# Optimization experiments

Hardware: AMD Instinct MI355X
Metric: run time of the kernel (lower is better)

## Reference

```python
import jax, jax.numpy as jnp
import numpy as np


def setup_inputs() -> dict:
    key = jax.random.key(0)
    ks = jax.random.split(key, 8)
    N, DIN, DOUT = 8192, 1024, 1024
    s = 1.0 / np.sqrt(DIN)
    return {
        "gAB": jax.random.normal(ks[0], (N, DIN), dtype=jnp.float32),
        "gAG": jax.random.normal(ks[1], (N, DIN), dtype=jnp.float32),
        "Wab": jax.random.normal(ks[2], (DIN, DOUT), dtype=jnp.float32) * s,
        "Wag": jax.random.normal(ks[3], (DIN, DOUT), dtype=jnp.float32) * s,
        "bab": jax.random.normal(ks[4], (DOUT,), dtype=jnp.float32) * 0.01,
        "bag": jax.random.normal(ks[5], (DOUT,), dtype=jnp.float32) * 0.01,
        "sAB": jax.random.normal(ks[6], (N, DOUT), dtype=jnp.float32),
        "sAG": jax.random.normal(ks[7], (N, DOUT), dtype=jnp.float32),
    }


def reference(gAB, gAG, Wab, Wag, bab, bag, sAB, sAG) -> jnp.ndarray:
    # project() per encoder (Linear): [N, DIN] @ [DIN, DOUT] + b
    pAB = gAB @ Wab + bab  # [N, DOUT]
    pAG = gAG @ Wag + bag  # [N, DOUT]
    # torch.diag(pAB @ pAG.T) == row-wise dot product (avoids O(N^2 d) waste)
    h1 = jnp.sum(pAB * pAG, axis=1, keepdims=True)  # [N, 1]
    h2 = jnp.sum(sAB * sAG, axis=1, keepdims=True)  # [N, 1]
    # mean over concatenated (h1, h2) columns, keepdim=True
    h = jnp.mean(jnp.concatenate([h1, h2], axis=1), axis=1, keepdims=True)  # [N, 1]
    return h
```

## Files before the change

kernel.cpp:

```cpp
#include <hip/hip_runtime.h>
#include <hip/hip_bf16.h>
#include <stdint.h>

typedef __attribute__((ext_vector_type(8))) short bf16x8;
typedef __attribute__((ext_vector_type(4))) float f32x4;

#define DIN 1024
#define NROWS 8192

__device__ __forceinline__ unsigned short f2bf(float f) {
    union { float f; unsigned u; } v; v.f = f;
    unsigned r = v.u + 0x7FFFu + ((v.u >> 16) & 1u);
    return (unsigned short)(r >> 16);
}

__device__ __forceinline__ int fswz(int r) { return (r ^ (r >> 2)) & 3; }

__device__ __forceinline__ size_t swz_byte(int R, int c) {
    return ((size_t)R * DIN + (size_t)(c & ~31)) * 2
         + (size_t)((((c >> 3) & 3) ^ fswz(R)) << 4)
         + (size_t)((c & 7) * 2);
}

__device__ __forceinline__ void gload_lds16(const void* g, void* l) {
    __builtin_amdgcn_global_load_lds(
        (const __attribute__((address_space(1))) unsigned*)g,
        (__attribute__((address_space(3))) unsigned*)l, 16, 0, 0);
}

__global__ __launch_bounds__(256) void prep_kernel(const float* __restrict__ Wab,
                                                   const float* __restrict__ Wag,
                                                   const float* __restrict__ bab,
                                                   const float* __restrict__ bag,
                                                   float* __restrict__ ws_f,
                                                   unsigned short* __restrict__ Whab,
                                                   unsigned short* __restrict__ Whag) {
    int b = blockIdx.x;
    int wave = threadIdx.x >> 6, lane = threadIdx.x & 63;
    if (b == 256) {
        if (wave == 0) {
            float acc = 0.f;
            for (int j = lane; j < DIN; j += 64) acc += bab[j] * bag[j];
            for (int off = 32; off; off >>= 1) acc += __shfl_xor(acc, off);
            if (lane == 0) ws_f[2048] = acc;
        }
        return;
    }
    int r = b * 4 + wave;
    int fr = fswz(r);
    {
        const float* wrow = Wab + (size_t)r * DIN;
        char* hrow = (char*)Whab + (size_t)r * DIN * 2;
        float acc = 0.f;
#pragma unroll
        for (int it = 0; it < 4; ++it) {
            int col = it * 256 + lane * 4;
            float4 w = *reinterpret_cast<const float4*>(wrow + col);
            float4 bv = *reinterpret_cast<const float4*>(bag + col);
            acc += w.x * bv.x + w.y * bv.y + w.z * bv.z + w.w * bv.w;
            ushort4 h; h.x = f2bf(w.x); h.y = f2bf(w.y); h.z = f2bf(w.z); h.w = f2bf(w.w);
            *reinterpret_cast<ushort4*>(hrow + (col & ~31) * 2 + ((((col >> 3) & 3) ^ fr) << 4) + (col & 7) * 2) = h;
        }
        for (int off = 32; off; off >>= 1) acc += __shfl_xor(acc, off);
        if (lane == 0) ws_f[r] = acc;
    }
    {
        const float* wrow = Wag + (size_t)r * DIN;
        char* hrow = (char*)Whag + (size_t)r * DIN * 2;
        float acc = 0.f;
#pragma unroll
        for (int it = 0; it < 4; ++it) {
            int col = it * 256 + lane * 4;
            float4 w = *reinterpret_cast<const float4*>(wrow + col);
            float4 bv = *reinterpret_cast<const float4*>(bab + col);
            acc += w.x * bv.x + w.y * bv.y + w.z * bv.z + w.w * bv.w;
            ushort4 h; h.x = f2bf(w.x); h.y = f2bf(w.y); h.z = f2bf(w.z); h.w = f2bf(w.w);
            *reinterpret_cast<ushort4*>(hrow + (col & ~31) * 2 + ((((col >> 3) & 3) ^ fr) << 4) + (col & 7) * 2) = h;
        }
        for (int off = 32; off; off >>= 1) acc += __shfl_xor(acc, off);
        if (lane == 0) ws_f[1024 + r] = acc;
    }
}

__global__ __launch_bounds__(256) void combo_kernel(const unsigned short* __restrict__ Whag,
                                                    const unsigned short* __restrict__ Whab,
                                                    unsigned short* __restrict__ Mt,
                                                    const float* __restrict__ gAB,
                                                    const float* __restrict__ sAB,
                                                    const float* __restrict__ sAG,
                                                    const float* __restrict__ ws_f,
                                                    unsigned short* __restrict__ gABh,
                                                    float* __restrict__ out,
                                                    int writecast) {
    __shared__ unsigned short sm[2][2][2][2048];
    int b = blockIdx.x;
    int tid = threadIdx.x, wave = tid >> 6, lane = tid & 63;

    if (b < 256) {
        int grp = wave >> 1, w2 = wave & 1;
        int kg = lane >> 4, cl = lane & 15;
        int br = b >> 4, bc = b & 15;
        int u = tid & 127;

        const char* Abase = (const char*)Whag + ((size_t)(br * 64) * DIN + grp * 512) * 2;
        const char* Bbase = (const char*)Whab + ((size_t)(bc * 64) * DIN + grp * 512) * 2;

        int offA[2], offB[4];
#pragma unroll
        for (int m = 0; m < 2; ++m) { int row = w2 * 32 + m * 16 + cl; offA[m] = row * 32 + ((kg ^ fswz(row)) << 3); }
#pragma unroll
        for (int n = 0; n < 4; ++n) { int row = n * 16 + cl; offB[n] = row * 32 + ((kg ^ fswz(row)) << 3); }

        f32x4 acc[2][4] = {};
#define STAGE_MT(buf, t)                                                            \
        _Pragma("unroll")                                                           \
        for (int it = 0; it < 2; ++it) {                                            \
            int un = u + it * 128, urow = un >> 2, uc = un & 3;                     \
            gload_lds16(Abase + (size_t)urow * 2048 + (t) * 64 + uc * 16,           \
                        &sm[grp][buf][0][un * 8]);                                  \
            gload_lds16(Bbase + (size_t)urow * 2048 + (t) * 64 + uc * 16,           \
                        &sm[grp][buf][1][un * 8]);                                  \
        }
        STAGE_MT(0, 0);
        for (int t = 0; t < 16; ++t) {
            int p = t & 1;
            __syncthreads();
            if (t < 15) { STAGE_MT(p ^ 1, t + 1); }
            bf16x8 af[2], bfr[4];
#pragma unroll
            for (int m = 0; m < 2; ++m) af[m] = *reinterpret_cast<const bf16x8*>(&sm[grp][p][0][offA[m]]);
#pragma unroll
            for (int n = 0; n < 4; ++n) bfr[n] = *reinterpret_cast<const bf16x8*>(&sm[grp][p][1][offB[n]]);
            __builtin_amdgcn_s_setprio(1);
#pragma unroll
            for (int m = 0; m < 2; ++m)
#pragma unroll
                for (int n = 0; n < 4; ++n)
                    acc[m][n] = __builtin_amdgcn_mfma_f32_16x16x32_bf16(af[m], bfr[n], acc[m][n], 0, 0, 0);
            __builtin_amdgcn_s_setprio(0);
        }
#undef STAGE_MT
        __syncthreads();
        float* red = (float*)sm;
        if (grp == 1) {
#pragma unroll
            for (int m = 0; m < 2; ++m)
#pragma unroll
                for (int n = 0; n < 4; ++n)
#pragma unroll
                    for (int j = 0; j < 4; ++j)
                        red[(w2 * 32 + m * 16 + kg * 4 + j) * 68 + n * 16 + cl] = acc[m][n][j];
        }
        __syncthreads();
        if (grp == 0) {
#pragma unroll
            for (int m = 0; m < 2; ++m)
#pragma unroll
                for (int n = 0; n < 4; ++n)
#pragma unroll
                    for (int j = 0; j < 4; ++j) {
                        int rl = w2 * 32 + m * 16 + kg * 4 + j, cll = n * 16 + cl;
                        float v = acc[m][n][j] + red[rl * 68 + cll];
                        int R = br * 64 + rl, C = bc * 64 + cll;
                        *(unsigned short*)((char*)Mt + swz_byte(R, C)) = f2bf(v);
                    }
        }
        return;
    }

    int row = (b - 256) * 4 + wave;
    const float* ga = gAB + (size_t)row * DIN;
    const float* sa = sAB + (size_t)row * DIN;
    const float* sg = sAG + (size_t)row * DIN;
    char* gh = (char*)gABh + (size_t)row * DIN * 2;
    int fr = fswz(row);
    float acc = 0.f;
#pragma unroll
    for (int cc = 0; cc < 4; ++cc) {
        int col = cc * 256 + lane * 4;
        float4 a = *reinterpret_cast<const float4*>(ga + col);
        float4 x = *reinterpret_cast<const float4*>(sa + col);
        float4 y = *reinterpret_cast<const float4*>(sg + col);
        float4 v = *reinterpret_cast<const float4*>(ws_f + col);
        acc += x.x * y.x + x.y * y.y + x.z * y.z + x.w * y.w;
        acc += a.x * v.x + a.y * v.y + a.z * v.z + a.w * v.w;
        if (writecast) {
            ushort4 h; h.x = f2bf(a.x); h.y = f2bf(a.y); h.z = f2bf(a.z); h.w = f2bf(a.w);
            *reinterpret_cast<ushort4*>(gh + (col & ~31) * 2 + ((((col >> 3) & 3) ^ fr) << 4) + (col & 7) * 2) = h;
        }
    }
#pragma unroll
    for (int off = 32; off; off >>= 1) acc += __shfl_xor(acc, off);
    if (lane == 0) out[row] = 0.5f * (acc + ws_f[2048]);
}

template <int PRECAST, int KSPLIT>
__global__ __launch_bounds__(256, 4) void gemm_kernel(const float* __restrict__ gAB,
                                                      const unsigned short* __restrict__ gABh,
                                                      const float* __restrict__ gAG,
                                                      const unsigned short* __restrict__ Mt,
                                                      const float* __restrict__ ws_f,
                                                      float* __restrict__ out) {
    __shared__ unsigned short lds_a[2][128 * 32];
    __shared__ unsigned short lds_b[2][128 * 32];
    constexpr int KLEN = DIN / KSPLIT;
    constexpr int NSTEP = KLEN / 32;
    int b = blockIdx.x;
    int x = b & 7, s = b >> 3;
    int rblk = x + 8 * (s & 7);
    int u2 = s >> 3;
    int ks = u2 & (KSPLIT - 1);
    int cblk = u2 / KSPLIT;
    int tid = threadIdx.x, wave = tid >> 6, lane = tid & 63;
    int wr = wave >> 1, wc = wave & 1;
    int kg = lane >> 4, cl = lane & 15;
    int row0 = rblk * 128, col0 = cblk * 128;

    int offA[4], offB[4];
#pragma unroll
    for (int m = 0; m < 4; ++m) { int row = wr * 64 + m * 16 + cl; offA[m] = row * 32 + ((kg ^ fswz(row)) << 3); }
#pragma unroll
    for (int n = 0; n < 4; ++n) { int row = wc * 64 + n * 16 + cl; offB[n] = row * 32 + ((kg ^ fswz(row)) << 3); }

    size_t kofs = (size_t)(ks * KLEN) * 2;
    const char* Ab = (const char*)gABh + (size_t)row0 * DIN * 2 + kofs;
    const char* Bb = (const char*)Mt + (size_t)col0 * DIN * 2 + kofs;
    int u0 = tid, u1 = tid + 256;
    size_t a0 = (size_t)(u0 >> 2) * (DIN * 2) + (u0 & 3) * 16;
    size_t a1 = (size_t)(u1 >> 2) * (DIN * 2) + (u1 & 3) * 16;

    f32x4 acc[4][4] = {};
    float4 ra[4];
    if (PRECAST) {
        gload_lds16(Ab + a0, (char*)&lds_a[0][0] + u0 * 16);
        gload_lds16(Ab + a1, (char*)&lds_a[0][0] + u1 * 16);
        gload_lds16(Bb + a0, (char*)&lds_b[0][0] + u0 * 16);
        gload_lds16(Bb + a1, (char*)&lds_b[0][0] + u1 * 16);

        for (int t = 0; t < NSTEP; ++t) {
            int p = t & 1;
            __syncthreads();
            if (t < NSTEP - 1) {
                gload_lds16(Ab + a0 + (t + 1) * 64, (char*)&lds_a[p ^ 1][0] + u0 * 16);
                gload_lds16(Ab + a1 + (t + 1) * 64, (char*)&lds_a[p ^ 1][0] + u1 * 16);
                gload_lds16(Bb + a0 + (t + 1) * 64, (char*)&lds_b[p ^ 1][0] + u0 * 16);
                gload_lds16(Bb + a1 + (t + 1) * 64, (char*)&lds_b[p ^ 1][0] + u1 * 16);
            }
            bf16x8 af[4], bfr[4];
#pragma unroll
            for (int m = 0; m < 4; ++m) af[m] = *reinterpret_cast<const bf16x8*>(&lds_a[p][offA[m]]);
#pragma unroll
            for (int n = 0; n < 4; ++n) bfr[n] = *reinterpret_cast<const bf16x8*>(&lds_b[p][offB[n]]);
            __builtin_amdgcn_s_setprio(1);
#pragma unroll
            for (int m = 0; m < 4; ++m)
#pragma unroll
                for (int n = 0; n < 4; ++n)
                    acc[m][n] = __builtin_amdgcn_mfma_f32_16x16x32_bf16(af[m], bfr[n], acc[m][n], 0, 0, 0);
            __builtin_amdgcn_s_setprio(0);
        }
    } else {
#pragma unroll
        for (int it = 0; it < 4; ++it) {
            int u = tid + it * 256;
            ra[it] = *reinterpret_cast<const float4*>(gAB + (size_t)(row0 + (u >> 3)) * DIN + ks * KLEN + (u & 7) * 4);
        }
#pragma unroll
        for (int it = 0; it < 4; ++it) {
            int u = tid + it * 256, row = u >> 3, c4 = u & 7;
            ushort4 h; h.x = f2bf(ra[it].x); h.y = f2bf(ra[it].y); h.z = f2bf(ra[it].z); h.w = f2bf(ra[it].w);
            *reinterpret_cast<ushort4*>((char*)&lds_a[0][0] + row * 64 + ((((c4 >> 1) ^ fswz(row))) << 4) + (c4 & 1) * 8) = h;
        }
        gload_lds16(Bb + a0, (char*)&lds_b[0][0] + u0 * 16);
        gload_lds16(Bb + a1, (char*)&lds_b[0][0] + u1 * 16);
        for (int t = 0; t < NSTEP; ++t) {
            int p = t & 1;
            __syncthreads();
            if (t < NSTEP - 1) {
#pragma unroll
                for (int it = 0; it < 4; ++it) {
                    int u = tid + it * 256;
                    ra[it] = *reinterpret_cast<const float4*>(gAB + (size_t)(row0 + (u >> 3)) * DIN + ks * KLEN + (t + 1) * 32 + (u & 7) * 4);
                }
                gload_lds16(Bb + a0 + (t + 1) * 64, (char*)&lds_b[p ^ 1][0] + u0 * 16);
                gload_lds16(Bb + a1 + (t + 1) * 64, (char*)&lds_b[p ^ 1][0] + u1 * 16);
            }
            bf16x8 af[4], bfr[4];
#pragma unroll
            for (int m = 0; m < 4; ++m) af[m] = *reinterpret_cast<const bf16x8*>(&lds_a[p][offA[m]]);
#pragma unroll
            for (int n = 0; n < 4; ++n) bfr[n] = *reinterpret_cast<const bf16x8*>(&lds_b[p][offB[n]]);
#pragma unroll
            for (int m = 0; m < 4; ++m)
#pragma unroll
                for (int n = 0; n < 4; ++n)
                    acc[m][n] = __builtin_amdgcn_mfma_f32_16x16x32_bf16(af[m], bfr[n], acc[m][n], 0, 0, 0);
            if (t < NSTEP - 1) {
#pragma unroll
                for (int it = 0; it < 4; ++it) {
                    int u = tid + it * 256, row = u >> 3, c4 = u & 7;
                    ushort4 h; h.x = f2bf(ra[it].x); h.y = f2bf(ra[it].y); h.z = f2bf(ra[it].z); h.w = f2bf(ra[it].w);
                    *reinterpret_cast<ushort4*>((char*)&lds_a[p ^ 1][0] + row * 64 + ((((c4 >> 1) ^ fswz(row))) << 4) + (c4 & 1) * 8) = h;
                }
            }
        }
    }

    const float* vag = ws_f + 1024;
#pragma unroll
    for (int m = 0; m < 4; ++m)
#pragma unroll
        for (int j = 0; j < 4; ++j) {
            int row = row0 + wr * 64 + m * 16 + kg * 4 + j;
            const float* gr = gAG + (size_t)row * DIN;
            float t = 0.f;
#pragma unroll
            for (int n = 0; n < 4; ++n) {
                int col = col0 + wc * 64 + n * 16 + cl;
                float addv = (ks == 0) ? vag[col] : 0.f;
                t += gr[col] * (acc[m][n][j] + addv);
            }
            t += __shfl_xor(t, 1);
            t += __shfl_xor(t, 2);
            t += __shfl_xor(t, 4);
            t += __shfl_xor(t, 8);
            if (cl == 0) atomicAdd(out + row, 0.5f * t);
        }
}

extern "C" void kernel_launch(void* const* d_in, const int* in_sizes, int n_in,
                              void* d_out, int out_size, void* d_ws, size_t ws_size,
                              hipStream_t stream) {
    const float* gAB = (const float*)d_in[0];
    const float* gAG = (const float*)d_in[1];
    const float* Wab = (const float*)d_in[2];
    const float* Wag = (const float*)d_in[3];
    const float* bab = (const float*)d_in[4];
    const float* bag = (const float*)d_in[5];
    const float* sAB = (const float*)d_in[6];
    const float* sAG = (const float*)d_in[7];
    float* out = (float*)d_out;

    float* ws_f = (float*)d_ws;
    char* base = (char*)d_ws + 16384;
    unsigned short* Mt = (unsigned short*)base;
    unsigned short* Whag = (unsigned short*)(base + (size_t)2 * 1024 * 1024);
    unsigned short* Whab = (unsigned short*)(base + (size_t)4 * 1024 * 1024);
    unsigned short* gABh = (unsigned short*)(base + (size_t)6 * 1024 * 1024);
    size_t need_full = 16384 + (size_t)22 * 1024 * 1024;
    int precast = (ws_size >= need_full) ? 1 : 0;

    prep_kernel<<<257, 256, 0, stream>>>(Wab, Wag, bab, bag, ws_f, Whab, Whag);
    combo_kernel<<<2304, 256, 0, stream>>>(Whag, Whab, Mt, gAB, sAB, sAG, ws_f, gABh, out, precast);
    if (precast)
        gemm_kernel<1, 2><<<1024, 256, 0, stream>>>(gAB, gABh, gAG, Mt, ws_f, out);
    else
        gemm_kernel<0, 2><<<1024, 256, 0, stream>>>(gAB, gABh, gAG, Mt, ws_f, out);
}
```

Measured before the change: 61.46 us.

## Use 256x256 GEMM tiles with 512 threads and 4-way K split

Replaces the 128x128, 256-thread, 2-way K-split GEMM on the precast path with a 256x256 tile kernel that uses 8 waves and splits K four ways, with 512 blocks. Each wave computes a 128x64 sub-tile, loading A fragments per m-row so they are reused across four B fragments. The goal is higher operand reuse per LDS and global byte and less redundant global traffic. In exchange, LDS per block doubles (64KB), accumulator register pressure rises, and the larger K split doubles the atomic adds into the output. The fallback path is refactored into a separate kernel with macros.

```diff
diff --git a/kernel.cpp b/kernel.cpp
--- a/kernel.cpp
+++ b/kernel.cpp
@@ -194,17 +194,103 @@
     if (lane == 0) out[row] = 0.5f * (acc + ws_f[2048]);
 }
 
-template <int PRECAST, int KSPLIT>
-__global__ __launch_bounds__(256, 4) void gemm_kernel(const float* __restrict__ gAB,
-                                                      const unsigned short* __restrict__ gABh,
-                                                      const float* __restrict__ gAG,
-                                                      const unsigned short* __restrict__ Mt,
-                                                      const float* __restrict__ ws_f,
-                                                      float* __restrict__ out) {
+__global__ __launch_bounds__(512, 4) void gemm256k4(const unsigned short* __restrict__ gABh,
+                                                    const float* __restrict__ gAG,
+                                                    const unsigned short* __restrict__ Mt,
+                                                    const float* __restrict__ ws_f,
+                                                    float* __restrict__ out) {
+    __shared__ unsigned short lds_a[2][256 * 32];
+    __shared__ unsigned short lds_b[2][256 * 32];
+    constexpr int NSTEP = 8;
+    int b = blockIdx.x;
+    int x = b & 7, s = b >> 3;
+    int rblk = x + 8 * (s & 3);
+    int rem = s >> 2;
+    int ks = rem & 3;
+    int cblk = rem >> 2;
+    int tid = threadIdx.x, wave = tid >> 6, lane = tid & 63;
+    int wr = wave >> 2, wc = wave & 3;
+    int kg = lane >> 4, cl = lane & 15;
+    int row0 = rblk * 256, col0 = cblk * 256;
+
+    const char* Ab = (const char*)gABh + (size_t)row0 * 2048 + ks * 512;
+    const char* Bb = (const char*)Mt + (size_t)col0 * 2048 + ks * 512;
+
+    int offA[8], offB[4];
+#pragma unroll
+    for (int m = 0; m < 8; ++m) { int row = wr * 128 + m * 16 + cl; offA[m] = row * 64 + ((kg ^ fswz(row)) << 4); }
+#pragma unroll
+    for (int n = 0; n < 4; ++n) { int row = wc * 64 + n * 16 + cl; offB[n] = row * 64 + ((kg ^ fswz(row)) << 4); }
+
+#define STAGE(buf, t) do {                                                          \
+    _Pragma("unroll")                                                               \
+    for (int it = 0; it < 2; ++it) {                                                \
+        int u = tid + it * 512;                                                     \
+        int row_ = u >> 2, c_ = u & 3;                                              \
+        gload_lds16(Ab + (size_t)row_ * 2048 + (t) * 64 + c_ * 16,                  \
+                    (char*)&lds_a[buf][0] + u * 16);                                \
+    }                                                                               \
+    _Pragma("unroll")                                                               \
+    for (int it = 0; it < 2; ++it) {                                                \
+        int u = tid + it * 512;                                                     \
+        int row_ = u >> 2, c_ = u & 3;                                              \
+        gload_lds16(Bb + (size_t)row_ * 2048 + (t) * 64 + c_ * 16,                  \
+                    (char*)&lds_b[buf][0] + u * 16);                                \
+    }                                                                               \
+} while (0)
+
+    f32x4 acc[8][4] = {};
+
+    STAGE(0, 0);
+    for (int t = 0; t < NSTEP; ++t) {
+        int p = t & 1;
+        __syncthreads();
+        if (t < NSTEP - 1) { STAGE(p ^ 1, t + 1); }
+        bf16x8 bfr[4];
+#pragma unroll
+        for (int n = 0; n < 4; ++n) bfr[n] = *reinterpret_cast<const bf16x8*>((char*)&lds_b[p][0] + offB[n]);
+#pragma unroll
+        for (int m = 0; m < 8; ++m) {
+            bf16x8 af = *reinterpret_cast<const bf16x8*>((char*)&lds_a[p][0] + offA[m]);
+            __builtin_amdgcn_s_setprio(1);
+#pragma unroll
+            for (int n = 0; n < 4; ++n)
+                acc[m][n] = __builtin_amdgcn_mfma_f32_16x16x32_bf16(af, bfr[n], acc[m][n], 0, 0, 0);
+            __builtin_amdgcn_s_setprio(0);
+        }
+    }
+#undef STAGE
+
+    const float* vag = ws_f + 1024;
+#pragma unroll
+    for (int m = 0; m < 8; ++m)
+#pragma unroll
+        for (int j = 0; j < 4; ++j) {
+            int row = row0 + wr * 128 + m * 16 + kg * 4 + j;
+            const float* gr = gAG + (size_t)row * DIN;
+            float tt = 0.f;
+#pragma unroll
+            for (int n = 0; n < 4; ++n) {
+                int col = col0 + wc * 64 + n * 16 + cl;
+                float addv = (ks == 0) ? vag[col] : 0.f;
+                tt += gr[col] * (acc[m][n][j] + addv);
+            }
+            tt += __shfl_xor(tt, 1);
+            tt += __shfl_xor(tt, 2);
+            tt += __shfl_xor(tt, 4);
+            tt += __shfl_xor(tt, 8);
+            if (cl == 0) atomicAdd(out + row, 0.5f * tt);
+        }
+}
+
+__global__ __launch_bounds__(256, 4) void gemm_fb(const float* __restrict__ gAB,
+                                                  const float* __restrict__ gAG,
+                                                  const unsigned short* __restrict__ Mt,
+                                                  const float* __restrict__ ws_f,
+                                                  float* __restrict__ out) {
     __shared__ unsigned short lds_a[2][128 * 32];
     __shared__ unsigned short lds_b[2][128 * 32];
-    constexpr int KLEN = DIN / KSPLIT;
-    constexpr int NSTEP = KLEN / 32;
+    constexpr int KSPLIT = 2, KLEN = DIN / KSPLIT, NSTEP = KLEN / 32;
     int b = blockIdx.x;
     int x = b & 7, s = b >> 3;
     int rblk = x + 8 * (s & 7);
@@ -218,94 +304,55 @@
 
     int offA[4], offB[4];
 #pragma unroll
-    for (int m = 0; m < 4; ++m) { int row = wr * 64 + m * 16 + cl; offA[m] = row * 32 + ((kg ^ fswz(row)) << 3); }
-#pragma unroll
-    for (int n = 0; n < 4; ++n) { int row = wc * 64 + n * 16 + cl; offB[n] = row * 32 + ((kg ^ fswz(row)) << 3); }
-
-    size_t kofs = (size_t)(ks * KLEN) * 2;
-    const char* Ab = (const char*)gABh + (size_t)row0 * DIN * 2 + kofs;
-    const char* Bb = (const char*)Mt + (size_t)col0 * DIN * 2 + kofs;
-    int u0 = tid, u1 = tid + 256;
-    size_t a0 = (size_t)(u0 >> 2) * (DIN * 2) + (u0 & 3) * 16;
-    size_t a1 = (size_t)(u1 >> 2) * (DIN * 2) + (u1 & 3) * 16;
+    for (int m = 0; m < 4; ++m) { int row = wr * 64 + m * 16 + cl; offA[m] = row * 64 + ((kg ^ fswz(row)) << 4); }
+#pragma unroll
+    for (int n = 0; n < 4; ++n) { int row = wc * 64 + n * 16 + cl; offB[n] = row * 64 + ((kg ^ fswz(row)) << 4); }
+
+    const float* Af = gAB + (size_t)row0 * DIN + ks * KLEN;
+    const char* Bb = (const char*)Mt + ((size_t)col0 * DIN + ks * KLEN) * 2;
 
     f32x4 acc[4][4] = {};
     float4 ra[4];
-    if (PRECAST) {
-        gload_lds16(Ab + a0, (char*)&lds_a[0][0] + u0 * 16);
-        gload_lds16(Ab + a1, (char*)&lds_a[0][0] + u1 * 16);
-        gload_lds16(Bb + a0, (char*)&lds_b[0][0] + u0 * 16);
-        gload_lds16(Bb + a1, (char*)&lds_b[0][0] + u1 * 16);
-
-        for (int t = 0; t < NSTEP; ++t) {
-            int p = t & 1;
-            __syncthreads();
-            if (t < NSTEP - 1) {
-                gload_lds16(Ab + a0 + (t + 1) * 64, (char*)&lds_a[p ^ 1][0] + u0 * 16);
-                gload_lds16(Ab + a1 + (t + 1) * 64, (char*)&lds_a[p ^ 1][0] + u1 * 16);
-                gload_lds16(Bb + a0 + (t + 1) * 64, (char*)&lds_b[p ^ 1][0] + u0 * 16);
-                gload_lds16(Bb + a1 + (t + 1) * 64, (char*)&lds_b[p ^ 1][0] + u1 * 16);
-            }
-            bf16x8 af[4], bfr[4];
-#pragma unroll
-            for (int m = 0; m < 4; ++m) af[m] = *reinterpret_cast<const bf16x8*>(&lds_a[p][offA[m]]);
-#pragma unroll
-            for (int n = 0; n < 4; ++n) bfr[n] = *reinterpret_cast<const bf16x8*>(&lds_b[p][offB[n]]);
-            __builtin_amdgcn_s_setprio(1);
-#pragma unroll
-            for (int m = 0; m < 4; ++m)
-#pragma unroll
-                for (int n = 0; n < 4; ++n)
-                    acc[m][n] = __builtin_amdgcn_mfma_f32_16x16x32_bf16(af[m], bfr[n], acc[m][n], 0, 0, 0);
-            __builtin_amdgcn_s_setprio(0);
-        }
-    } else {
-#pragma unroll
-        for (int it = 0; it < 4; ++it) {
-            int u = tid + it * 256;
-            ra[it] = *reinterpret_cast<const float4*>(gAB + (size_t)(row0 + (u >> 3)) * DIN + ks * KLEN + (u & 7) * 4);
-        }
-#pragma unroll
-        for (int it = 0; it < 4; ++it) {
-            int u = tid + it * 256, row = u >> 3, c4 = u & 7;
-            ushort4 h; h.x = f2bf(ra[it].x); h.y = f2bf(ra[it].y); h.z = f2bf(ra[it].z); h.w = f2bf(ra[it].w);
-            *reinterpret_cast<ushort4*>((char*)&lds_a[0][0] + row * 64 + ((((c4 >> 1) ^ fswz(row))) << 4) + (c4 & 1) * 8) = h;
-        }
-        gload_lds16(Bb + a0, (char*)&lds_b[0][0] + u0 * 16);
-        gload_lds16(Bb + a1, (char*)&lds_b[0][0] + u1 * 16);
-        for (int t = 0; t < NSTEP; ++t) {
-            int p = t & 1;
-            __syncthreads();
-            if (t < NSTEP - 1) {
-#pragma unroll
-                for (int it = 0; it < 4; ++it) {
-                    int u = tid + it * 256;
-                    ra[it] = *reinterpret_cast<const float4*>(gAB + (size_t)(row0 + (u >> 3)) * DIN + ks * KLEN + (t + 1) * 32 + (u & 7) * 4);
-                }
-                gload_lds16(Bb + a0 + (t + 1) * 64, (char*)&lds_b[p ^ 1][0] + u0 * 16);
-                gload_lds16(Bb + a1 + (t + 1) * 64, (char*)&lds_b[p ^ 1][0] + u1 * 16);
-            }
-            bf16x8 af[4], bfr[4];
-#pragma unroll
-            for (int m = 0; m < 4; ++m) af[m] = *reinterpret_cast<const bf16x8*>(&lds_a[p][offA[m]]);
-#pragma unroll
-            for (int n = 0; n < 4; ++n) bfr[n] = *reinterpret_cast<const bf16x8*>(&lds_b[p][offB[n]]);
-#pragma unroll
-            for (int m = 0; m < 4; ++m)
-#pragma unroll
-                for (int n = 0; n < 4; ++n)
-                    acc[m][n] = __builtin_amdgcn_mfma_f32_16x16x32_bf16(af[m], bfr[n], acc[m][n], 0, 0, 0);
-            if (t < NSTEP - 1) {
-#pragma unroll
-                for (int it = 0; it < 4; ++it) {
-                    int u = tid + it * 256, row = u >> 3, c4 = u & 7;
-                    ushort4 h; h.x = f2bf(ra[it].x); h.y = f2bf(ra[it].y); h.z = f2bf(ra[it].z); h.w = f2bf(ra[it].w);
-                    *reinterpret_cast<ushort4*>((char*)&lds_a[p ^ 1][0] + row * 64 + ((((c4 >> 1) ^ fswz(row))) << 4) + (c4 & 1) * 8) = h;
-                }
-            }
-        }
-    }
-
+#define STAGE_A(buf, t)                                                             \
+    _Pragma("unroll")                                                               \
+    for (int it = 0; it < 4; ++it) {                                                \
+        int u = tid + it * 256, row_ = u >> 3, c4 = u & 7;                          \
+        ra[it] = *reinterpret_cast<const float4*>(Af + (size_t)row_ * DIN + (t) * 32 + c4 * 4); \
+    }                                                                               \
+    _Pragma("unroll")                                                               \
+    for (int it = 0; it < 4; ++it) {                                                \
+        int u = tid + it * 256, row_ = u >> 3, c4 = u & 7;                          \
+        ushort4 h; h.x = f2bf(ra[it].x); h.y = f2bf(ra[it].y); h.z = f2bf(ra[it].z); h.w = f2bf(ra[it].w); \
+        *reinterpret_cast<ushort4*>((char*)&lds_a[buf][0] + row_ * 64 +             \
+                                    (((c4 >> 1) ^ fswz(row_)) << 4) + (c4 & 1) * 8) = h; \
+    }
+#define STAGE_Bm(buf, t)                                                            \
+    _Pragma("unroll")                                                               \
+    for (int it = 0; it < 2; ++it) {                                                \
+        int u = tid + it * 256, row_ = u >> 2, c_ = u & 3;                          \
+        gload_lds16(Bb + (size_t)row_ * 2048 + (t) * 64 + c_ * 16,                  \
+                    (char*)&lds_b[buf][0] + u * 16);                                \
+    }
+    STAGE_A(0, 0);
+    STAGE_Bm(0, 0);
+    for (int t = 0; t < NSTEP; ++t) {
+        int p = t & 1;
+        __syncthreads();
+        if (t < NSTEP - 1) { STAGE_Bm(p ^ 1, t + 1); }
+        bf16x8 af[4], bfr[4];
+#pragma unroll
+        for (int m = 0; m < 4; ++m) af[m] = *reinterpret_cast<const bf16x8*>((char*)&lds_a[p][0] + offA[m]);
+#pragma unroll
+        for (int n = 0; n < 4; ++n) bfr[n] = *reinterpret_cast<const bf16x8*>((char*)&lds_b[p][0] + offB[n]);
+#pragma unroll
+        for (int m = 0; m < 4; ++m)
+#pragma unroll
+            for (int n = 0; n < 4; ++n)
+                acc[m][n] = __builtin_amdgcn_mfma_f32_16x16x32_bf16(af[m], bfr[n], acc[m][n], 0, 0, 0);
+        if (t < NSTEP - 1) { STAGE_A(p ^ 1, t + 1); }
+    }
+#undef STAGE_A
+#undef STAGE_Bm
     const float* vag = ws_f + 1024;
 #pragma unroll
     for (int m = 0; m < 4; ++m)
@@ -313,18 +360,18 @@
         for (int j = 0; j < 4; ++j) {
             int row = row0 + wr * 64 + m * 16 + kg * 4 + j;
             const float* gr = gAG + (size_t)row * DIN;
-            float t = 0.f;
+            float tt = 0.f;
 #pragma unroll
             for (int n = 0; n < 4; ++n) {
                 int col = col0 + wc * 64 + n * 16 + cl;
                 float addv = (ks == 0) ? vag[col] : 0.f;
-                t += gr[col] * (acc[m][n][j] + addv);
+                tt += gr[col] * (acc[m][n][j] + addv);
             }
-            t += __shfl_xor(t, 1);
-            t += __shfl_xor(t, 2);
-            t += __shfl_xor(t, 4);
-            t += __shfl_xor(t, 8);
-            if (cl == 0) atomicAdd(out + row, 0.5f * t);
+            tt += __shfl_xor(tt, 1);
+            tt += __shfl_xor(tt, 2);
+            tt += __shfl_xor(tt, 4);
+            tt += __shfl_xor(tt, 8);
+            if (cl == 0) atomicAdd(out + row, 0.5f * tt);
         }
 }
 
@@ -353,7 +400,7 @@
     prep_kernel<<<257, 256, 0, stream>>>(Wab, Wag, bab, bag, ws_f, Whab, Whag);
     combo_kernel<<<2304, 256, 0, stream>>>(Whag, Whab, Mt, gAB, sAB, sAG, ws_f, gABh, out, precast);
     if (precast)
-        gemm_kernel<1, 2><<<1024, 256, 0, stream>>>(gAB, gABh, gAG, Mt, ws_f, out);
+        gemm256k4<<<512, 512, 0, stream>>>(gABh, gAG, Mt, ws_f, out);
     else
-        gemm_kernel<0, 2><<<1024, 256, 0, stream>>>(gAB, gABh, gAG, Mt, ws_f, out);
-}
+        gemm_fb<<<1024, 256, 0, stream>>>(gAB, gAG, Mt, ws_f, out);
+}
```

Result: slower. 151.0 us (+145.6%).
